# Kernel optimization log

Measured on AMD Instinct MI355X. Metric: run time of the kernel, lower is better.

## Reference

```python
import jax, jax.numpy as jnp
import numpy as np

B, H = 4096, 200
NU, NV = 100000, 100000
DU, DV = 64, 64


def setup_inputs() -> dict:
    key = jax.random.key(0)
    ks = jax.random.split(key, 16)
    s = 0.05
    return {
        "nodes": jax.random.randint(ks[0], (B,), 0, NU),
        "history_uv": jax.random.randint(ks[1], (B, H), 0, NV),
        "history_r": jax.random.uniform(ks[2], (B, H), dtype=jnp.float32),
        "u2e_w": jax.random.normal(ks[3], (NU, DU), dtype=jnp.float32) * s,
        "v2e_w": jax.random.normal(ks[4], (NV, DV), dtype=jnp.float32) * s,
        "w_r1_w": jax.random.normal(ks[5], (DV, DV + 1), dtype=jnp.float32) * s,
        "w_r1_b": jax.random.normal(ks[6], (DV,), dtype=jnp.float32) * s,
        "w_r2_w": jax.random.normal(ks[7], (DV, DV), dtype=jnp.float32) * s,
        "w_r2_b": jax.random.normal(ks[8], (DV,), dtype=jnp.float32) * s,
        "att1_w": jax.random.normal(ks[9], (DV, DV + DU), dtype=jnp.float32) * s,
        "att1_b": jax.random.normal(ks[10], (DV,), dtype=jnp.float32) * s,
        "att2_w": jax.random.normal(ks[11], (DV, DV), dtype=jnp.float32) * s,
        "att2_b": jax.random.normal(ks[12], (DV,), dtype=jnp.float32) * s,
        "att3_w": jax.random.normal(ks[13], (1, DV), dtype=jnp.float32) * s,
        "att3_b": jax.random.normal(ks[14], (1,), dtype=jnp.float32) * s,
    }


def reference(nodes, history_uv, history_r, u2e_w, v2e_w,
              w_r1_w, w_r1_b, w_r2_w, w_r2_b,
              att1_w, att1_b, att2_w, att2_b, att3_w, att3_b):
    # Gather: e_uv [B,H,DV], uv_rep [B,DU]
    e_uv = v2e_w[history_uv]
    uv_rep = u2e_w[nodes]
    # x = cat(e_uv, e_r) -> two Linear+ReLU (dropout is identity in eval)
    x = jnp.concatenate([e_uv, history_r[..., None]], axis=-1)  # [B,H,DV+1]
    x = jax.nn.relu(jnp.einsum('bhi,oi->bho', x, w_r1_w) + w_r1_b)
    o_history = jax.nn.relu(jnp.einsum('bhi,oi->bho', x, w_r2_w) + w_r2_b)  # [B,H,DV]
    # Attention MLP over cat(o_history, u_rep broadcast to neighbors)
    u_rep_b = jnp.broadcast_to(uv_rep[:, None, :], (o_history.shape[0], o_history.shape[1], uv_rep.shape[-1]))
    a = jnp.concatenate([o_history, u_rep_b], axis=-1)  # [B,H,DV+DU]
    a = jax.nn.relu(jnp.einsum('bhi,oi->bho', a, att1_w) + att1_b)
    a = jax.nn.relu(jnp.einsum('bhi,oi->bho', a, att2_w) + att2_b)
    logits = jnp.einsum('bhi,oi->bho', a, att3_w) + att3_b  # [B,H,1]
    att = jax.nn.softmax(logits, axis=1)  # softmax over neighbor axis
    # Attention-weighted neighbor sum: [B,DV]
    to_feats = jnp.sum(o_history * att, axis=1)
    return to_feats
```

## Files before the change

kernel.cpp:

```cpp
#include <hip/hip_runtime.h>
#include <hip/hip_bf16.h>
#include <math.h>

#define Bn 4096
#define Hn 200

typedef float f32x16 __attribute__((ext_vector_type(16)));
typedef short short8 __attribute__((ext_vector_type(8)));
typedef __bf16 bh8 __attribute__((ext_vector_type(8)));
typedef unsigned int u32;

#define TABW     3200000
#define BIAS_OFF 10240
#define WR_OFF   10496
#define AT3_OFF  10560
#define WTOT     10624

union Frag { u32 w[4]; short8 s; };

__device__ __forceinline__ u32 pk2(float a, float b){
    union { __hip_bfloat162 bf; u32 u; } cv;
    cv.bf = __float22bfloat162_rn(make_float2(a, b));
    return cv.u;
}

template <typename T>
__device__ __forceinline__ auto mfma_sel(T a, T b, f32x16 c, int)
    -> decltype(__builtin_amdgcn_mfma_f32_32x32x16_bf16(a, b, c, 0, 0, 0)) {
    return __builtin_amdgcn_mfma_f32_32x32x16_bf16(a, b, c, 0, 0, 0);
}
template <typename T>
__device__ __forceinline__ f32x16 mfma_sel(T a, T b, f32x16 c, long) {
    return __builtin_amdgcn_mfma_f32_32x32x16_bf16(
        __builtin_bit_cast(bh8, a), __builtin_bit_cast(bh8, b), c, 0, 0, 0);
}

__device__ __forceinline__ f32x16 mfma16v(uint4 a, const u32* b, f32x16 c){
    Frag fa, fb;
    fa.w[0] = a.x; fa.w[1] = a.y; fa.w[2] = a.z; fa.w[3] = a.w;
#pragma unroll
    for (int i = 0; i < 4; ++i) fb.w[i] = b[i];
    return mfma_sel(fa.s, fb.s, c, 0);
}
__device__ __forceinline__ f32x16 mfma16w(uint4 a, uint4 b, f32x16 c){
    Frag fa, fb;
    fa.w[0] = a.x; fa.w[1] = a.y; fa.w[2] = a.z; fa.w[3] = a.w;
    fb.w[0] = b.x; fb.w[1] = b.y; fb.w[2] = b.z; fb.w[3] = b.w;
    return mfma_sel(fa.s, fb.s, c, 0);
}

__device__ __forceinline__ void dtile_to_b(f32x16 d, u32 ow[2][4]){
    u32 p0 = pk2(d[0], d[1]),   p1 = pk2(d[2], d[3]);
    u32 p2 = pk2(d[4], d[5]),   p3 = pk2(d[6], d[7]);
    u32 p4 = pk2(d[8], d[9]),   p5 = pk2(d[10], d[11]);
    u32 p6 = pk2(d[12], d[13]), p7 = pk2(d[14], d[15]);
    auto r0 = __builtin_amdgcn_permlane32_swap(p0, p2, false, false);
    ow[0][0] = (u32)r0[0]; ow[0][2] = (u32)r0[1];
    auto r1 = __builtin_amdgcn_permlane32_swap(p1, p3, false, false);
    ow[0][1] = (u32)r1[0]; ow[0][3] = (u32)r1[1];
    auto r2 = __builtin_amdgcn_permlane32_swap(p4, p6, false, false);
    ow[1][0] = (u32)r2[0]; ow[1][2] = (u32)r2[1];
    auto r3 = __builtin_amdgcn_permlane32_swap(p5, p7, false, false);
    ow[1][1] = (u32)r3[0]; ow[1][3] = (u32)r3[1];
}

__device__ __forceinline__ void load_f16(const float* p, float bf[16]){
    const float4* q = (const float4*)p;
    float4 a = q[0], b = q[1], c = q[2], d = q[3];
    bf[0]=a.x; bf[1]=a.y; bf[2]=a.z; bf[3]=a.w;
    bf[4]=b.x; bf[5]=b.y; bf[6]=b.z; bf[7]=b.w;
    bf[8]=c.x; bf[9]=c.y; bf[10]=c.z; bf[11]=c.w;
    bf[12]=d.x; bf[13]=d.y; bf[14]=d.z; bf[15]=d.w;
}

__global__ __launch_bounds__(256) void prep(
    const float* __restrict__ v2e_w,
    const float* __restrict__ w_r1_w, const float* __restrict__ w_r1_b,
    const float* __restrict__ w_r2_w, const float* __restrict__ w_r2_b,
    const float* __restrict__ att1_w, const float* __restrict__ att1_b,
    const float* __restrict__ att2_w, const float* __restrict__ att2_b,
    const float* __restrict__ att3_w,
    u32* __restrict__ ws, int table_n, int woff)
{
    const int g = blockIdx.x * 256 + threadIdx.x;
    if (g < table_n) {
        const float4* src = (const float4*)v2e_w + (size_t)g * 2;
        float4 a = src[0], b = src[1];
        uint4 o; o.x = pk2(a.x, a.y); o.y = pk2(a.z, a.w);
                 o.z = pk2(b.x, b.y); o.w = pk2(b.z, b.w);
        ((uint4*)ws)[g] = o;
        return;
    }
    int q = g - table_n;
    u32* wbase = ws + woff;
    if (q < 2560) {
        const int c = q >> 6, l = q & 63, lo = l & 31, h = l >> 5;
        const float* W; int ldw, ft, kc, colb;
        if (c < 8)       { W = w_r1_w; ldw = 65;  ft = c >> 2;       kc = c & 3;       colb = 0; }
        else if (c < 16) { W = w_r2_w; ldw = 64;  ft = (c - 8) >> 2; kc = (c - 8) & 3; colb = 0; }
        else if (c < 32) { int c3 = c - 16; W = att1_w; ldw = 128; ft = c3 >> 3; kc = c3 & 3; colb = 64 * ((c3 >> 2) & 1); }
        else             { int c4 = c - 32; W = att2_w; ldw = 64;  ft = c4 >> 2; kc = c4 & 3; colb = 0; }
        const float* p = W + (32 * ft + lo) * ldw + colb + 16 * kc + 8 * h;
        uint4 o; o.x = pk2(p[0], p[1]); o.y = pk2(p[2], p[3]);
                 o.z = pk2(p[4], p[5]); o.w = pk2(p[6], p[7]);
        ((uint4*)wbase)[c * 64 + l] = o;
        return;
    }
    q -= 2560;
    if (q < 256) {
        const int layer = q >> 6, ft = (q >> 5) & 1, h = (q >> 4) & 1, rg = q & 15;
        const float* bp = layer == 0 ? w_r1_b : layer == 1 ? w_r2_b : layer == 2 ? att1_b : att2_b;
        ((float*)wbase)[BIAS_OFF + q] = bp[32 * ft + (rg & 3) + 8 * (rg >> 2) + 4 * h];
        return;
    }
    q -= 256;
    if (q < 64) {
        const int ft = (q >> 5) & 1, h = (q >> 4) & 1, rg = q & 15;
        ((float*)wbase)[WR_OFF + q] = w_r1_w[(32 * ft + (rg & 3) + 8 * (rg >> 2) + 4 * h) * 65 + 64];
        return;
    }
    q -= 64;
    if (q < 64) {
        const int ft = (q >> 5) & 1, h = (q >> 4) & 1, rg = q & 15;
        ((float*)wbase)[AT3_OFF + q] = att3_w[32 * ft + (rg & 3) + 8 * (rg >> 2) + 4 * h];
    }
}

template<int USE_TAB>
__global__ __launch_bounds__(256, 3) void uv_agg(
    const int* __restrict__ nodes,
    const int* __restrict__ history_uv,
    const float* __restrict__ history_r,
    const float* __restrict__ u2e_w,
    const float* __restrict__ v2e_w,
    const float* __restrict__ att3_b,
    const u32* __restrict__ ws,
    float* __restrict__ out)
{
    const int b  = blockIdx.x;
    const int t  = threadIdx.x;
    const int w  = t >> 6;
    const int l  = t & 63;
    const int lo = l & 31;
    const int h  = l >> 5;

    constexpr int woff = USE_TAB ? TABW : 0;
    const uint4* WF = (const uint4*)(ws + woff);
    const float* F  = (const float*)(ws + woff);

    __shared__ u32   oh_lds[Hn * 32];
    __shared__ float att_red[256];
    __shared__ float swax[4], ssum[4];
    __shared__ u32   u_lds[32];

    if (t < 32) {
        const int node = nodes[b];
        const float2 uv = ((const float2*)(u2e_w + (size_t)node * 64))[t];
        u_lds[t] = pk2(uv.x, uv.y);
    }

    const int hb  = b * Hn;
    const int m0  = 64 * w + lo;
    const int m1  = m0 + 32;
    const int mi0 = m0 < Hn ? m0 : Hn - 1;
    const int mi1 = m1 < Hn ? m1 : Hn - 1;
    const int vidx0 = history_uv[hb + mi0];
    const int vidx1 = history_uv[hb + mi1];
    const float r0  = history_r[hb + mi0];
    const float r1  = history_r[hb + mi1];

    u32 eB[2][4][4];
    if constexpr (USE_TAB) {
        const uint4* t0 = (const uint4*)ws + (size_t)vidx0 * 8;
        const uint4* t1 = (const uint4*)ws + (size_t)vidx1 * 8;
#pragma unroll
        for (int kc = 0; kc < 4; ++kc){
            uint4 x = t0[2 * kc + h];
            eB[0][kc][0] = x.x; eB[0][kc][1] = x.y; eB[0][kc][2] = x.z; eB[0][kc][3] = x.w;
            uint4 y = t1[2 * kc + h];
            eB[1][kc][0] = y.x; eB[1][kc][1] = y.y; eB[1][kc][2] = y.z; eB[1][kc][3] = y.w;
        }
    } else {
        const float4* p0 = (const float4*)(v2e_w + (size_t)vidx0 * 64);
        const float4* p1 = (const float4*)(v2e_w + (size_t)vidx1 * 64);
#pragma unroll
        for (int kc = 0; kc < 4; ++kc){
            float4 a = p0[4*kc + 2*h], c = p0[4*kc + 2*h + 1];
            eB[0][kc][0] = pk2(a.x, a.y); eB[0][kc][1] = pk2(a.z, a.w);
            eB[0][kc][2] = pk2(c.x, c.y); eB[0][kc][3] = pk2(c.z, c.w);
            a = p1[4*kc + 2*h]; c = p1[4*kc + 2*h + 1];
            eB[1][kc][0] = pk2(a.x, a.y); eB[1][kc][1] = pk2(a.z, a.w);
            eB[1][kc][2] = pk2(c.x, c.y); eB[1][kc][3] = pk2(c.z, c.w);
        }
    }

    u32 x1B[2][4][4];
#pragma unroll
    for (int ft = 0; ft < 2; ++ft){
        uint4 W[4];
#pragma unroll
        for (int kc = 0; kc < 4; ++kc) W[kc] = WF[(ft*4 + kc)*64 + l];
        float bf[16], wr[16];
        load_f16(F + BIAS_OFF + ft*32 + h*16, bf);
        load_f16(F + WR_OFF  + ft*32 + h*16, wr);
#pragma unroll
        for (int rt = 0; rt < 2; ++rt){
            const float rv = rt ? r1 : r0;
            f32x16 a;
#pragma unroll
            for (int rg = 0; rg < 16; ++rg) a[rg] = fmaf(wr[rg], rv, bf[rg]);
#pragma unroll
            for (int kc = 0; kc < 4; ++kc) a = mfma16v(W[kc], eB[rt][kc], a);
#pragma unroll
            for (int i2 = 0; i2 < 16; ++i2) a[i2] = fmaxf(a[i2], 0.f);
            u32 ow[2][4];
            dtile_to_b(a, ow);
#pragma unroll
            for (int v = 0; v < 4; ++v){ x1B[rt][2*ft][v] = ow[0][v]; x1B[rt][2*ft+1][v] = ow[1][v]; }
        }
    }

    u32 ohB[2][4][4];
#pragma unroll
    for (int ft = 0; ft < 2; ++ft){
        uint4 W[4];
#pragma unroll
        for (int kc = 0; kc < 4; ++kc) W[kc] = WF[(8 + ft*4 + kc)*64 + l];
        float bf[16];
        load_f16(F + BIAS_OFF + 64 + ft*32 + h*16, bf);
#pragma unroll
        for (int rt = 0; rt < 2; ++rt){
            f32x16 a;
#pragma unroll
            for (int rg = 0; rg < 16; ++rg) a[rg] = bf[rg];
#pragma unroll
            for (int kc = 0; kc < 4; ++kc) a = mfma16v(W[kc], x1B[rt][kc], a);
#pragma unroll
            for (int i2 = 0; i2 < 16; ++i2) a[i2] = fmaxf(a[i2], 0.f);
            u32 ow[2][4];
            dtile_to_b(a, ow);
#pragma unroll
            for (int v = 0; v < 4; ++v){ ohB[rt][2*ft][v] = ow[0][v]; ohB[rt][2*ft+1][v] = ow[1][v]; }
        }
    }

#pragma unroll
    for (int kc = 0; kc < 4; ++kc)
#pragma unroll
        for (int rt = 0; rt < 2; ++rt)
#pragma unroll
            for (int v = 0; v < 4; ++v){
                const int c = 8 * kc + 4 * h + v;
                const int m = 64 * w + 32 * rt + lo;
                if (m < Hn) oh_lds[m * 32 + (c ^ lo)] = ohB[rt][kc][v];
            }

    __syncthreads();

    u32 a1B[2][4][4];
#pragma unroll
    for (int ft = 0; ft < 2; ++ft){
        uint4 W[4], W2[4];
#pragma unroll
        for (int kc = 0; kc < 4; ++kc) W[kc]  = WF[(16 + ft*8 + kc)*64 + l];
#pragma unroll
        for (int kc = 0; kc < 4; ++kc) W2[kc] = WF[(16 + ft*8 + 4 + kc)*64 + l];
        float bf[16];
        load_f16(F + BIAS_OFF + 128 + ft*32 + h*16, bf);
#pragma unroll
        for (int rt = 0; rt < 2; ++rt){
            f32x16 a;
#pragma unroll
            for (int rg = 0; rg < 16; ++rg) a[rg] = bf[rg];
#pragma unroll
            for (int kc = 0; kc < 4; ++kc) a = mfma16v(W[kc], ohB[rt][kc], a);
#pragma unroll
            for (int kc = 0; kc < 4; ++kc){
                const int j = 8 * kc + 4 * h;
                uint4 uu = make_uint4(u_lds[j], u_lds[j+1], u_lds[j+2], u_lds[j+3]);
                a = mfma16w(W2[kc], uu, a);
            }
#pragma unroll
            for (int i2 = 0; i2 < 16; ++i2) a[i2] = fmaxf(a[i2], 0.f);
            u32 ow[2][4];
            dtile_to_b(a, ow);
#pragma unroll
            for (int v = 0; v < 4; ++v){ a1B[rt][2*ft][v] = ow[0][v]; a1B[rt][2*ft+1][v] = ow[1][v]; }
        }
    }

    float lgp0 = 0.f, lgp1 = 0.f;
#pragma unroll
    for (int ft = 0; ft < 2; ++ft){
        uint4 W[4];
#pragma unroll
        for (int kc = 0; kc < 4; ++kc) W[kc] = WF[(32 + ft*4 + kc)*64 + l];
        float bf[16], a3[16];
        load_f16(F + BIAS_OFF + 192 + ft*32 + h*16, bf);
        load_f16(F + AT3_OFF + ft*32 + h*16, a3);
#pragma unroll
        for (int rt = 0; rt < 2; ++rt){
            f32x16 a;
#pragma unroll
            for (int rg = 0; rg < 16; ++rg) a[rg] = bf[rg];
#pragma unroll
            for (int kc = 0; kc < 4; ++kc) a = mfma16v(W[kc], a1B[rt][kc], a);
            float p = 0.f;
#pragma unroll
            for (int rg = 0; rg < 16; ++rg) p = fmaf(fmaxf(a[rg], 0.f), a3[rg], p);
            if (rt) lgp1 += p; else lgp0 += p;
        }
    }
    const float b3 = att3_b[0];
    float lg0 = lgp0 + __shfl_xor(lgp0, 32, 64) + b3;
    float lg1 = lgp1 + __shfl_xor(lgp1, 32, 64) + b3;
    if (m0 >= Hn) lg0 = -1e30f;
    if (m1 >= Hn) lg1 = -1e30f;

    float mx = fmaxf(lg0, lg1);
#pragma unroll
    for (int d = 16; d >= 1; d >>= 1) mx = fmaxf(mx, __shfl_xor(mx, d, 64));
    if (l == 0) swax[w] = mx;
    __syncthreads();
    mx = fmaxf(fmaxf(swax[0], swax[1]), fmaxf(swax[2], swax[3]));
    const float e0 = exp2f((lg0 - mx) * 1.4426950408889634f);
    const float e1 = exp2f((lg1 - mx) * 1.4426950408889634f);
    float sm = e0 + e1;
#pragma unroll
    for (int d = 16; d >= 1; d >>= 1) sm += __shfl_xor(sm, d, 64);
    if (l == 0) ssum[w] = sm;
    __syncthreads();
    const float inv = 1.f / (ssum[0] + ssum[1] + ssum[2] + ssum[3]);
    att_red[64 * w + 32 * h + lo] = (h ? e1 : e0) * inv;
    __syncthreads();

    float s0 = 0.f, s1 = 0.f;
#pragma unroll 8
    for (int i = 0; i < 32; ++i){
        const int m  = 64 * w + 32 * h + i;
        const int mi = m < Hn ? m : Hn - 1;
        const u32 wv = oh_lds[mi * 32 + (lo ^ (mi & 31))];
        const float av = att_red[m];
        s0 = fmaf(__uint_as_float(wv << 16), av, s0);
        s1 = fmaf(__uint_as_float(wv & 0xffff0000u), av, s1);
    }
    s0 += __shfl_xor(s0, 32, 64);
    s1 += __shfl_xor(s1, 32, 64);
    __syncthreads();
    if (l < 32){ att_red[w * 64 + 2 * lo] = s0; att_red[w * 64 + 2 * lo + 1] = s1; }
    __syncthreads();
    if (t < 64)
        out[b * 64 + t] = att_red[t] + att_red[64 + t] + att_red[128 + t] + att_red[192 + t];
}

extern "C" void kernel_launch(void* const* d_in, const int* in_sizes, int n_in,
                              void* d_out, int out_size, void* d_ws, size_t ws_size,
                              hipStream_t stream) {
    u32* ws = (u32*)d_ws;
    const size_t need_tab = (size_t)(TABW + WTOT) * 4;
    const int use_tab = (ws_size >= need_tab) ? 1 : 0;
    const int woff    = use_tab ? TABW : 0;
    const int table_n = use_tab ? 800000 : 0;
    const int prep_threads = table_n + 2944;
    const int prep_blocks  = (prep_threads + 255) / 256;

    prep<<<prep_blocks, 256, 0, stream>>>(
        (const float*)d_in[4],
        (const float*)d_in[5],  (const float*)d_in[6],
        (const float*)d_in[7],  (const float*)d_in[8],
        (const float*)d_in[9],  (const float*)d_in[10],
        (const float*)d_in[11], (const float*)d_in[12],
        (const float*)d_in[13],
        ws, table_n, woff);

    if (use_tab) {
        uv_agg<1><<<Bn, 256, 0, stream>>>(
            (const int*)d_in[0], (const int*)d_in[1], (const float*)d_in[2],
            (const float*)d_in[3], (const float*)d_in[4], (const float*)d_in[14],
            ws, (float*)d_out);
    } else {
        uv_agg<0><<<Bn, 256, 0, stream>>>(
            (const int*)d_in[0], (const int*)d_in[1], (const float*)d_in[2],
            (const float*)d_in[3], (const float*)d_in[4], (const float*)d_in[14],
            ws, (float*)d_out);
    }
}
```

Baseline: 86.46 us.

## Split neighbor rows across seven waves with one MFMA row-tile each

Each block now uses 7 waves of 64 threads, with every wave processing a single 32-neighbor tile instead of two, so 200 neighbors pad to 224 instead of 256 rows. Register arrays shrink to one tile, and the launch bound targets higher occupancy. Weight fragments are reloaded per tile instead of reused across two tiles, and the reductions grow to seven partials.

```diff
diff --git a/kernel.cpp b/kernel.cpp
--- a/kernel.cpp
+++ b/kernel.cpp
@@ -4,6 +4,8 @@
 
 #define Bn 4096
 #define Hn 200
+#define NW 7
+#define NT (NW * 64)
 
 typedef float f32x16 __attribute__((ext_vector_type(16)));
 typedef short short8 __attribute__((ext_vector_type(8)));
@@ -16,8 +18,6 @@
 #define AT3_OFF  10560
 #define WTOT     10624
 
-union Frag { u32 w[4]; short8 s; };
-
 __device__ __forceinline__ u32 pk2(float a, float b){
     union { __hip_bfloat162 bf; u32 u; } cv;
     cv.bf = __float22bfloat162_rn(make_float2(a, b));
@@ -34,43 +34,21 @@
     return __builtin_amdgcn_mfma_f32_32x32x16_bf16(
         __builtin_bit_cast(bh8, a), __builtin_bit_cast(bh8, b), c, 0, 0, 0);
 }
-
-__device__ __forceinline__ f32x16 mfma16v(uint4 a, const u32* b, f32x16 c){
-    Frag fa, fb;
-    fa.w[0] = a.x; fa.w[1] = a.y; fa.w[2] = a.z; fa.w[3] = a.w;
-#pragma unroll
-    for (int i = 0; i < 4; ++i) fb.w[i] = b[i];
-    return mfma_sel(fa.s, fb.s, c, 0);
-}
-__device__ __forceinline__ f32x16 mfma16w(uint4 a, uint4 b, f32x16 c){
-    Frag fa, fb;
-    fa.w[0] = a.x; fa.w[1] = a.y; fa.w[2] = a.z; fa.w[3] = a.w;
-    fb.w[0] = b.x; fb.w[1] = b.y; fb.w[2] = b.z; fb.w[3] = b.w;
-    return mfma_sel(fa.s, fb.s, c, 0);
-}
-
-__device__ __forceinline__ void dtile_to_b(f32x16 d, u32 ow[2][4]){
+__device__ __forceinline__ f32x16 mfma_u4(uint4 a, uint4 b, f32x16 c){
+    return mfma_sel(__builtin_bit_cast(short8, a), __builtin_bit_cast(short8, b), c, 0);
+}
+
+__device__ __forceinline__ void dtile_to_b(f32x16 d, uint4& b0, uint4& b1){
     u32 p0 = pk2(d[0], d[1]),   p1 = pk2(d[2], d[3]);
     u32 p2 = pk2(d[4], d[5]),   p3 = pk2(d[6], d[7]);
     u32 p4 = pk2(d[8], d[9]),   p5 = pk2(d[10], d[11]);
     u32 p6 = pk2(d[12], d[13]), p7 = pk2(d[14], d[15]);
     auto r0 = __builtin_amdgcn_permlane32_swap(p0, p2, false, false);
-    ow[0][0] = (u32)r0[0]; ow[0][2] = (u32)r0[1];
     auto r1 = __builtin_amdgcn_permlane32_swap(p1, p3, false, false);
-    ow[0][1] = (u32)r1[0]; ow[0][3] = (u32)r1[1];
     auto r2 = __builtin_amdgcn_permlane32_swap(p4, p6, false, false);
-    ow[1][0] = (u32)r2[0]; ow[1][2] = (u32)r2[1];
     auto r3 = __builtin_amdgcn_permlane32_swap(p5, p7, false, false);
-    ow[1][1] = (u32)r3[0]; ow[1][3] = (u32)r3[1];
-}
-
-__device__ __forceinline__ void load_f16(const float* p, float bf[16]){
-    const float4* q = (const float4*)p;
-    float4 a = q[0], b = q[1], c = q[2], d = q[3];
-    bf[0]=a.x; bf[1]=a.y; bf[2]=a.z; bf[3]=a.w;
-    bf[4]=b.x; bf[5]=b.y; bf[6]=b.z; bf[7]=b.w;
-    bf[8]=c.x; bf[9]=c.y; bf[10]=c.z; bf[11]=c.w;
-    bf[12]=d.x; bf[13]=d.y; bf[14]=d.z; bf[15]=d.w;
+    b0 = make_uint4((u32)r0[0], (u32)r1[0], (u32)r0[1], (u32)r1[1]);
+    b1 = make_uint4((u32)r2[0], (u32)r3[0], (u32)r2[1], (u32)r3[1]);
 }
 
 __global__ __launch_bounds__(256) void prep(
@@ -127,7 +105,7 @@
 }
 
 template<int USE_TAB>
-__global__ __launch_bounds__(256, 3) void uv_agg(
+__global__ __launch_bounds__(NT, 7) void uv_agg(
     const int* __restrict__ nodes,
     const int* __restrict__ history_uv,
     const float* __restrict__ history_r,
@@ -149,208 +127,177 @@
     const float* F  = (const float*)(ws + woff);
 
     __shared__ u32   oh_lds[Hn * 32];
-    __shared__ float att_red[256];
-    __shared__ float swax[4], ssum[4];
+    __shared__ float att_lds[NW * 32];
+    __shared__ float red[NW][64];
+    __shared__ float swax[NW], ssum[NW];
     __shared__ u32   u_lds[32];
 
     if (t < 32) {
-        const int node = nodes[b];
-        const float2 uv = ((const float2*)(u2e_w + (size_t)node * 64))[t];
+        const float2 uv = ((const float2*)(u2e_w + (size_t)nodes[b] * 64))[t];
         u_lds[t] = pk2(uv.x, uv.y);
     }
 
-    const int hb  = b * Hn;
-    const int m0  = 64 * w + lo;
-    const int m1  = m0 + 32;
-    const int mi0 = m0 < Hn ? m0 : Hn - 1;
-    const int mi1 = m1 < Hn ? m1 : Hn - 1;
-    const int vidx0 = history_uv[hb + mi0];
-    const int vidx1 = history_uv[hb + mi1];
-    const float r0  = history_r[hb + mi0];
-    const float r1  = history_r[hb + mi1];
-
-    u32 eB[2][4][4];
+    const int m  = 32 * w + lo;
+    const int mi = m < Hn ? m : Hn - 1;
+    const int   vidx = history_uv[b * Hn + mi];
+    const float r    = history_r[b * Hn + mi];
+
+    uint4 eB[4];
     if constexpr (USE_TAB) {
-        const uint4* t0 = (const uint4*)ws + (size_t)vidx0 * 8;
-        const uint4* t1 = (const uint4*)ws + (size_t)vidx1 * 8;
-#pragma unroll
-        for (int kc = 0; kc < 4; ++kc){
-            uint4 x = t0[2 * kc + h];
-            eB[0][kc][0] = x.x; eB[0][kc][1] = x.y; eB[0][kc][2] = x.z; eB[0][kc][3] = x.w;
-            uint4 y = t1[2 * kc + h];
-            eB[1][kc][0] = y.x; eB[1][kc][1] = y.y; eB[1][kc][2] = y.z; eB[1][kc][3] = y.w;
-        }
+        const uint4* tp = (const uint4*)ws + (size_t)vidx * 8;
+#pragma unroll
+        for (int kc = 0; kc < 4; ++kc) eB[kc] = tp[2 * kc + h];
     } else {
-        const float4* p0 = (const float4*)(v2e_w + (size_t)vidx0 * 64);
-        const float4* p1 = (const float4*)(v2e_w + (size_t)vidx1 * 64);
+        const float4* p0 = (const float4*)(v2e_w + (size_t)vidx * 64);
 #pragma unroll
         for (int kc = 0; kc < 4; ++kc){
             float4 a = p0[4*kc + 2*h], c = p0[4*kc + 2*h + 1];
-            eB[0][kc][0] = pk2(a.x, a.y); eB[0][kc][1] = pk2(a.z, a.w);
-            eB[0][kc][2] = pk2(c.x, c.y); eB[0][kc][3] = pk2(c.z, c.w);
-            a = p1[4*kc + 2*h]; c = p1[4*kc + 2*h + 1];
-            eB[1][kc][0] = pk2(a.x, a.y); eB[1][kc][1] = pk2(a.z, a.w);
-            eB[1][kc][2] = pk2(c.x, c.y); eB[1][kc][3] = pk2(c.z, c.w);
-        }
-    }
-
-    u32 x1B[2][4][4];
+            eB[kc] = make_uint4(pk2(a.x, a.y), pk2(a.z, a.w), pk2(c.x, c.y), pk2(c.z, c.w));
+        }
+    }
+
+    uint4 x1B[4];
 #pragma unroll
     for (int ft = 0; ft < 2; ++ft){
-        uint4 W[4];
-#pragma unroll
-        for (int kc = 0; kc < 4; ++kc) W[kc] = WF[(ft*4 + kc)*64 + l];
-        float bf[16], wr[16];
-        load_f16(F + BIAS_OFF + ft*32 + h*16, bf);
-        load_f16(F + WR_OFF  + ft*32 + h*16, wr);
-#pragma unroll
-        for (int rt = 0; rt < 2; ++rt){
-            const float rv = rt ? r1 : r0;
-            f32x16 a;
-#pragma unroll
-            for (int rg = 0; rg < 16; ++rg) a[rg] = fmaf(wr[rg], rv, bf[rg]);
-#pragma unroll
-            for (int kc = 0; kc < 4; ++kc) a = mfma16v(W[kc], eB[rt][kc], a);
-#pragma unroll
-            for (int i2 = 0; i2 < 16; ++i2) a[i2] = fmaxf(a[i2], 0.f);
-            u32 ow[2][4];
-            dtile_to_b(a, ow);
-#pragma unroll
-            for (int v = 0; v < 4; ++v){ x1B[rt][2*ft][v] = ow[0][v]; x1B[rt][2*ft+1][v] = ow[1][v]; }
-        }
-    }
-
-    u32 ohB[2][4][4];
+        f32x16 a;
+        {
+            const float4* bp = (const float4*)(F + BIAS_OFF + ft*32 + h*16);
+            const float4* wp = (const float4*)(F + WR_OFF  + ft*32 + h*16);
+#pragma unroll
+            for (int i = 0; i < 4; ++i){
+                float4 bv = bp[i], wv = wp[i];
+                a[4*i+0] = fmaf(wv.x, r, bv.x); a[4*i+1] = fmaf(wv.y, r, bv.y);
+                a[4*i+2] = fmaf(wv.z, r, bv.z); a[4*i+3] = fmaf(wv.w, r, bv.w);
+            }
+        }
+#pragma unroll
+        for (int kc = 0; kc < 4; ++kc) a = mfma_u4(WF[(ft*4 + kc)*64 + l], eB[kc], a);
+#pragma unroll
+        for (int i = 0; i < 16; ++i) a[i] = fmaxf(a[i], 0.f);
+        dtile_to_b(a, x1B[2*ft], x1B[2*ft+1]);
+    }
+
+    uint4 ohB[4];
 #pragma unroll
     for (int ft = 0; ft < 2; ++ft){
-        uint4 W[4];
-#pragma unroll
-        for (int kc = 0; kc < 4; ++kc) W[kc] = WF[(8 + ft*4 + kc)*64 + l];
-        float bf[16];
-        load_f16(F + BIAS_OFF + 64 + ft*32 + h*16, bf);
-#pragma unroll
-        for (int rt = 0; rt < 2; ++rt){
-            f32x16 a;
-#pragma unroll
-            for (int rg = 0; rg < 16; ++rg) a[rg] = bf[rg];
-#pragma unroll
-            for (int kc = 0; kc < 4; ++kc) a = mfma16v(W[kc], x1B[rt][kc], a);
-#pragma unroll
-            for (int i2 = 0; i2 < 16; ++i2) a[i2] = fmaxf(a[i2], 0.f);
-            u32 ow[2][4];
-            dtile_to_b(a, ow);
-#pragma unroll
-            for (int v = 0; v < 4; ++v){ ohB[rt][2*ft][v] = ow[0][v]; ohB[rt][2*ft+1][v] = ow[1][v]; }
-        }
-    }
-
-#pragma unroll
-    for (int kc = 0; kc < 4; ++kc)
-#pragma unroll
-        for (int rt = 0; rt < 2; ++rt)
+        f32x16 a;
+        {
+            const float4* bp = (const float4*)(F + BIAS_OFF + 64 + ft*32 + h*16);
+#pragma unroll
+            for (int i = 0; i < 4; ++i){
+                float4 bv = bp[i];
+                a[4*i+0] = bv.x; a[4*i+1] = bv.y; a[4*i+2] = bv.z; a[4*i+3] = bv.w;
+            }
+        }
+#pragma unroll
+        for (int kc = 0; kc < 4; ++kc) a = mfma_u4(WF[(8 + ft*4 + kc)*64 + l], x1B[kc], a);
+#pragma unroll
+        for (int i = 0; i < 16; ++i) a[i] = fmaxf(a[i], 0.f);
+        dtile_to_b(a, ohB[2*ft], ohB[2*ft+1]);
+    }
+
+    if (m < Hn) {
+#pragma unroll
+        for (int kc = 0; kc < 4; ++kc){
+            const u32* pw = (const u32*)&ohB[kc];
 #pragma unroll
             for (int v = 0; v < 4; ++v){
                 const int c = 8 * kc + 4 * h + v;
-                const int m = 64 * w + 32 * rt + lo;
-                if (m < Hn) oh_lds[m * 32 + (c ^ lo)] = ohB[rt][kc][v];
-            }
-
-    __syncthreads();
-
-    u32 a1B[2][4][4];
+                oh_lds[m * 32 + (c ^ lo)] = pw[v];
+            }
+        }
+    }
+
+    __syncthreads();
+
+    uint4 a1B[4];
 #pragma unroll
     for (int ft = 0; ft < 2; ++ft){
-        uint4 W[4], W2[4];
-#pragma unroll
-        for (int kc = 0; kc < 4; ++kc) W[kc]  = WF[(16 + ft*8 + kc)*64 + l];
-#pragma unroll
-        for (int kc = 0; kc < 4; ++kc) W2[kc] = WF[(16 + ft*8 + 4 + kc)*64 + l];
-        float bf[16];
-        load_f16(F + BIAS_OFF + 128 + ft*32 + h*16, bf);
-#pragma unroll
-        for (int rt = 0; rt < 2; ++rt){
-            f32x16 a;
-#pragma unroll
-            for (int rg = 0; rg < 16; ++rg) a[rg] = bf[rg];
-#pragma unroll
-            for (int kc = 0; kc < 4; ++kc) a = mfma16v(W[kc], ohB[rt][kc], a);
-#pragma unroll
-            for (int kc = 0; kc < 4; ++kc){
-                const int j = 8 * kc + 4 * h;
-                uint4 uu = make_uint4(u_lds[j], u_lds[j+1], u_lds[j+2], u_lds[j+3]);
-                a = mfma16w(W2[kc], uu, a);
-            }
-#pragma unroll
-            for (int i2 = 0; i2 < 16; ++i2) a[i2] = fmaxf(a[i2], 0.f);
-            u32 ow[2][4];
-            dtile_to_b(a, ow);
-#pragma unroll
-            for (int v = 0; v < 4; ++v){ a1B[rt][2*ft][v] = ow[0][v]; a1B[rt][2*ft+1][v] = ow[1][v]; }
-        }
-    }
-
-    float lgp0 = 0.f, lgp1 = 0.f;
+        f32x16 a;
+        {
+            const float4* bp = (const float4*)(F + BIAS_OFF + 128 + ft*32 + h*16);
+#pragma unroll
+            for (int i = 0; i < 4; ++i){
+                float4 bv = bp[i];
+                a[4*i+0] = bv.x; a[4*i+1] = bv.y; a[4*i+2] = bv.z; a[4*i+3] = bv.w;
+            }
+        }
+#pragma unroll
+        for (int kc = 0; kc < 4; ++kc) a = mfma_u4(WF[(16 + ft*8 + kc)*64 + l], ohB[kc], a);
+#pragma unroll
+        for (int kc = 0; kc < 4; ++kc){
+            const int j = 8 * kc + 4 * h;
+            uint4 uu = make_uint4(u_lds[j], u_lds[j+1], u_lds[j+2], u_lds[j+3]);
+            a = mfma_u4(WF[(16 + ft*8 + 4 + kc)*64 + l], uu, a);
+        }
+#pragma unroll
+        for (int i = 0; i < 16; ++i) a[i] = fmaxf(a[i], 0.f);
+        dtile_to_b(a, a1B[2*ft], a1B[2*ft+1]);
+    }
+
+    float lgp = 0.f;
 #pragma unroll
     for (int ft = 0; ft < 2; ++ft){
-        uint4 W[4];
-#pragma unroll
-        for (int kc = 0; kc < 4; ++kc) W[kc] = WF[(32 + ft*4 + kc)*64 + l];
-        float bf[16], a3[16];
-        load_f16(F + BIAS_OFF + 192 + ft*32 + h*16, bf);
-        load_f16(F + AT3_OFF + ft*32 + h*16, a3);
-#pragma unroll
-        for (int rt = 0; rt < 2; ++rt){
-            f32x16 a;
-#pragma unroll
-            for (int rg = 0; rg < 16; ++rg) a[rg] = bf[rg];
-#pragma unroll
-            for (int kc = 0; kc < 4; ++kc) a = mfma16v(W[kc], a1B[rt][kc], a);
-            float p = 0.f;
-#pragma unroll
-            for (int rg = 0; rg < 16; ++rg) p = fmaf(fmaxf(a[rg], 0.f), a3[rg], p);
-            if (rt) lgp1 += p; else lgp0 += p;
-        }
-    }
-    const float b3 = att3_b[0];
-    float lg0 = lgp0 + __shfl_xor(lgp0, 32, 64) + b3;
-    float lg1 = lgp1 + __shfl_xor(lgp1, 32, 64) + b3;
-    if (m0 >= Hn) lg0 = -1e30f;
-    if (m1 >= Hn) lg1 = -1e30f;
-
-    float mx = fmaxf(lg0, lg1);
+        f32x16 a;
+        float a3[16];
+        {
+            const float4* bp = (const float4*)(F + BIAS_OFF + 192 + ft*32 + h*16);
+            const float4* ap = (const float4*)(F + AT3_OFF + ft*32 + h*16);
+#pragma unroll
+            for (int i = 0; i < 4; ++i){
+                float4 bv = bp[i], av = ap[i];
+                a[4*i+0] = bv.x; a[4*i+1] = bv.y; a[4*i+2] = bv.z; a[4*i+3] = bv.w;
+                a3[4*i+0] = av.x; a3[4*i+1] = av.y; a3[4*i+2] = av.z; a3[4*i+3] = av.w;
+            }
+        }
+#pragma unroll
+        for (int kc = 0; kc < 4; ++kc) a = mfma_u4(WF[(32 + ft*4 + kc)*64 + l], a1B[kc], a);
+#pragma unroll
+        for (int rg = 0; rg < 16; ++rg) lgp = fmaf(fmaxf(a[rg], 0.f), a3[rg], lgp);
+    }
+    float lg = lgp + __shfl_xor(lgp, 32, 64) + att3_b[0];
+    if (m >= Hn) lg = -1e30f;
+
+    float mx = lg;
 #pragma unroll
     for (int d = 16; d >= 1; d >>= 1) mx = fmaxf(mx, __shfl_xor(mx, d, 64));
     if (l == 0) swax[w] = mx;
     __syncthreads();
-    mx = fmaxf(fmaxf(swax[0], swax[1]), fmaxf(swax[2], swax[3]));
-    const float e0 = exp2f((lg0 - mx) * 1.4426950408889634f);
-    const float e1 = exp2f((lg1 - mx) * 1.4426950408889634f);
-    float sm = e0 + e1;
+    mx = swax[0];
+#pragma unroll
+    for (int i = 1; i < NW; ++i) mx = fmaxf(mx, swax[i]);
+    const float e = exp2f((lg - mx) * 1.4426950408889634f);
+    float sm = e;
 #pragma unroll
     for (int d = 16; d >= 1; d >>= 1) sm += __shfl_xor(sm, d, 64);
     if (l == 0) ssum[w] = sm;
     __syncthreads();
-    const float inv = 1.f / (ssum[0] + ssum[1] + ssum[2] + ssum[3]);
-    att_red[64 * w + 32 * h + lo] = (h ? e1 : e0) * inv;
+    float tot = ssum[0];
+#pragma unroll
+    for (int i = 1; i < NW; ++i) tot += ssum[i];
+    if (h == 0) att_lds[m] = e / tot;
     __syncthreads();
 
     float s0 = 0.f, s1 = 0.f;
-#pragma unroll 8
-    for (int i = 0; i < 32; ++i){
-        const int m  = 64 * w + 32 * h + i;
-        const int mi = m < Hn ? m : Hn - 1;
-        const u32 wv = oh_lds[mi * 32 + (lo ^ (mi & 31))];
-        const float av = att_red[m];
+#pragma unroll
+    for (int i = 0; i < 16; ++i){
+        const int row = 32 * w + 16 * h + i;
+        const int ri  = row < Hn ? row : Hn - 1;
+        const u32 wv  = oh_lds[ri * 32 + (lo ^ (ri & 31))];
+        const float av = att_lds[row];
         s0 = fmaf(__uint_as_float(wv << 16), av, s0);
         s1 = fmaf(__uint_as_float(wv & 0xffff0000u), av, s1);
     }
     s0 += __shfl_xor(s0, 32, 64);
     s1 += __shfl_xor(s1, 32, 64);
-    __syncthreads();
-    if (l < 32){ att_red[w * 64 + 2 * lo] = s0; att_red[w * 64 + 2 * lo + 1] = s1; }
-    __syncthreads();
-    if (t < 64)
-        out[b * 64 + t] = att_red[t] + att_red[64 + t] + att_red[128 + t] + att_red[192 + t];
+    if (l < 32){ red[w][2 * lo] = s0; red[w][2 * lo + 1] = s1; }
+    __syncthreads();
+    if (t < 64){
+        float o = red[0][t];
+#pragma unroll
+        for (int i = 1; i < NW; ++i) o += red[i][t];
+        out[b * 64 + t] = o;
+    }
 }
 
 extern "C" void kernel_launch(void* const* d_in, const int* in_sizes, int n_in,
@@ -374,12 +321,12 @@
         ws, table_n, woff);
 
     if (use_tab) {
-        uv_agg<1><<<Bn, 256, 0, stream>>>(
+        uv_agg<1><<<Bn, NT, 0, stream>>>(
             (const int*)d_in[0], (const int*)d_in[1], (const float*)d_in[2],
             (const float*)d_in[3], (const float*)d_in[4], (const float*)d_in[14],
             ws, (float*)d_out);
     } else {
-        uv_agg<0><<<Bn, 256, 0, stream>>>(
+        uv_agg<0><<<Bn, NT, 0, stream>>>(
             (const int*)d_in[0], (const int*)d_in[1], (const float*)d_in[2],
             (const float*)d_in[3], (const float*)d_in[4], (const float*)d_in[14],
             ws, (float*)d_out);
```

Result: slower. 117.2 us (+35.6%).
